# Performance work log

Measured on AMD Instinct MI355X. Metric: run time of the kernel, lower is better.

The kernel has to match this reference:

```python
import jax, jax.numpy as jnp
import numpy as np

B, T = 16, 1024
EMBED, HIDDEN = 128, 256
NUM_CLASSES, NUM_LABELS = 8000, 100


def setup_inputs() -> dict:
    key = jax.random.key(0)
    ks = jax.random.split(key, 9)
    s_in = 1.0 / np.sqrt(HIDDEN)  # PyTorch LSTMCell init: U(-1/sqrt(H), 1/sqrt(H))
    return {
        "x": jax.random.randint(ks[0], (B, T, 2), 0, NUM_LABELS, dtype=jnp.int64),
        "embed_x_w": jax.random.uniform(ks[1], (NUM_CLASSES, EMBED), jnp.float32, -0.1, 0.1),
        "embed_label_w": jax.random.uniform(ks[2], (NUM_LABELS, EMBED), jnp.float32, -0.1, 0.1),
        "W_ih": jax.random.uniform(ks[3], (4 * HIDDEN, 2 * EMBED), jnp.float32, -s_in, s_in),
        "W_hh": jax.random.uniform(ks[4], (4 * HIDDEN, HIDDEN), jnp.float32, -s_in, s_in),
        "b_ih": jax.random.uniform(ks[5], (4 * HIDDEN,), jnp.float32, -s_in, s_in),
        "b_hh": jax.random.uniform(ks[6], (4 * HIDDEN,), jnp.float32, -s_in, s_in),
        "fc_w": jax.random.uniform(ks[7], (NUM_CLASSES, HIDDEN), jnp.float32, -s_in, s_in),
        "fc_b": jax.random.uniform(ks[8], (NUM_CLASSES,), jnp.float32, -s_in, s_in),
    }


def _lstm_forward(x, embed_x_w, embed_label_w, W_ih, W_hh, b_ih, b_hh, fc_w, fc_b):
    H = W_hh.shape[1]
    # embedding lookups + concat: [B, T, 2E]
    x_emb = embed_x_w[x[:, :, 0]]
    l_emb = embed_label_w[x[:, :, 1]]
    inp = jnp.concatenate([x_emb, l_emb], axis=-1)
    # precompute input projection for all timesteps: [T, B, 4H]
    x_proj = jnp.einsum("bte,ge->tbg", inp, W_ih) + b_ih + b_hh

    def step(carry, xp_t):
        h, c = carry
        gates = xp_t + h @ W_hh.T  # [B, 4H]
        i = jax.nn.sigmoid(gates[:, 0 * H:1 * H])
        f = jax.nn.sigmoid(gates[:, 1 * H:2 * H])
        g = jnp.tanh(gates[:, 2 * H:3 * H])
        o = jax.nn.sigmoid(gates[:, 3 * H:4 * H])
        c_new = f * c + i * g
        h_new = o * jnp.tanh(c_new)
        return (h_new, c_new), h_new

    bsz = x.shape[0]
    h0 = jnp.zeros((bsz, H), x_proj.dtype)
    c0 = jnp.zeros((bsz, H), x_proj.dtype)
    _, hs = jax.lax.scan(step, (h0, c0), x_proj)  # hs: [T, B, H]
    hs = jnp.transpose(hs, (1, 0, 2))  # [B, T, H]
    return jnp.einsum("bth,ch->btc", hs, fc_w) + fc_b  # [B, T, C]


def reference(x, embed_x_w, embed_label_w, W_ih, W_hh, b_ih, b_hh, fc_w, fc_b):
    return _lstm_forward(x, embed_x_w, embed_label_w, W_ih, W_hh, b_ih, b_hh, fc_w, fc_b)
```

## Files before the change

### kernel.cpp

```cpp
#include <hip/hip_runtime.h>
#include <hip/hip_bf16.h>
#include <stdint.h>

#define B_ 16
#define T_ 1024
#define EMBED_ 128
#define HID_ 256
#define G4_ 1024
#define NC_ 8000
#define M_ (B_*T_)

typedef short bf16x8 __attribute__((ext_vector_type(8)));
typedef float f32x4 __attribute__((ext_vector_type(4)));

#if defined(__has_builtin)
#if __has_builtin(__builtin_amdgcn_sdot4)
#define SDOT4(a,b,c) __builtin_amdgcn_sdot4((a),(b),(c),false)
#endif
#endif
#ifndef SDOT4
__device__ __forceinline__ int sdot4_sw(int a, int b, int c) {
    c += (int)(signed char)(a)       * (int)(signed char)(b);
    c += (int)(signed char)(a >> 8)  * (int)(signed char)(b >> 8);
    c += (int)(signed char)(a >> 16) * (int)(signed char)(b >> 16);
    c += (int)(signed char)(a >> 24) * (int)(signed char)(b >> 24);
    return c;
}
#define SDOT4(a,b,c) sdot4_sw((a),(b),(c))
#endif

__device__ __forceinline__ float sigmoid_f(float x) {
    float e = __expf(-x);
    return __builtin_amdgcn_rcpf(1.f + e);
}

__global__ void embed_kernel(const int* __restrict__ x,
                             const float* __restrict__ ew,
                             const float* __restrict__ lw,
                             __hip_bfloat16* __restrict__ inp) {
    int m = blockIdx.x;
    int e = threadIdx.x;
    int i0 = x[2 * m];
    int i1 = x[2 * m + 1];
    float v = (e < EMBED_) ? ew[i0 * EMBED_ + e] : lw[i1 * EMBED_ + (e - EMBED_)];
    inp[m * 256 + e] = __float2bfloat16(v);
}

__global__ void f2bf_kernel(const float* __restrict__ in,
                            __hip_bfloat16* __restrict__ out, int n) {
    int i = blockIdx.x * blockDim.x + threadIdx.x;
    if (i < n) out[i] = __float2bfloat16(in[i]);
}

__global__ void quant_whh_kernel(const float* __restrict__ whh,
                                 int* __restrict__ wq, float* __restrict__ wscale) {
    int r = blockIdx.x;
    int lane = threadIdx.x;
    float4 v = ((const float4*)(whh + r * HID_))[lane];
    float m = fmaxf(fmaxf(fabsf(v.x), fabsf(v.y)), fmaxf(fabsf(v.z), fabsf(v.w)));
    #pragma unroll
    for (int off = 32; off; off >>= 1) m = fmaxf(m, __shfl_xor(m, off, 64));
    m = fmaxf(m, 1e-20f);
    float inv = 127.f / m;
    int q0 = __float2int_rn(v.x * inv) & 255;
    int q1 = __float2int_rn(v.y * inv) & 255;
    int q2 = __float2int_rn(v.z * inv) & 255;
    int q3 = __float2int_rn(v.w * inv) & 255;
    wq[r * 64 + lane] = q0 | (q1 << 8) | (q2 << 16) | (q3 << 24);
    if (lane == 0) wscale[r] = m * (1.f / 127.f);
}

__global__ __launch_bounds__(256, 4)
void gemm_bf16_kernel(const __hip_bfloat16* __restrict__ A,
                      const __hip_bfloat16* __restrict__ Bm,
                      const float* __restrict__ bias1,
                      const float* __restrict__ bias2,
                      float* __restrict__ C,
                      int N, int out_mode) {
    __shared__ short As[64][136];
    __shared__ short Bs[64][136];
    const int tid = threadIdx.x;
    const int m0 = blockIdx.y * 64;
    const int n0 = blockIdx.x * 64;
    const int w = tid >> 6;
    const int lane = tid & 63;
    const int l15 = lane & 15;
    const int q = lane >> 4;

    f32x4 zero4 = {0.f, 0.f, 0.f, 0.f};
    f32x4 acc[4] = {zero4, zero4, zero4, zero4};

    const int r = tid >> 2;
    const int cbase = tid & 3;

    for (int ko = 0; ko < 256; ko += 128) {
        #pragma unroll
        for (int i = 0; i < 4; ++i) {
            int c = cbase + (i << 2);
            uint4 av = ((const uint4*)A)[(size_t)(m0 + r) * 32 + (ko >> 3) + c];
            *((uint4*)&As[r][c * 8]) = av;
            uint4 bv = ((const uint4*)Bm)[(size_t)(n0 + r) * 32 + (ko >> 3) + c];
            *((uint4*)&Bs[r][c * 8]) = bv;
        }
        __syncthreads();
        #pragma unroll
        for (int kc = 0; kc < 4; ++kc) {
            bf16x8 af = *((const bf16x8*)&As[w * 16 + l15][kc * 32 + q * 8]);
            #pragma unroll
            for (int nt = 0; nt < 4; ++nt) {
                bf16x8 bfr = *((const bf16x8*)&Bs[nt * 16 + l15][kc * 32 + q * 8]);
                acc[nt] = __builtin_amdgcn_mfma_f32_16x16x32_bf16(af, bfr, acc[nt], 0, 0, 0);
            }
        }
        __syncthreads();
    }

    #pragma unroll
    for (int nt = 0; nt < 4; ++nt) {
        int n = n0 + nt * 16 + l15;
        float bsum = bias1[n] + (bias2 ? bias2[n] : 0.f);
        #pragma unroll
        for (int rg = 0; rg < 4; ++rg) {
            int m = m0 + w * 16 + q * 4 + rg;
            float val = acc[nt][rg] + bsum;
            if (out_mode == 0) {
                C[(size_t)m * N + n] = val;
            } else {
                int t = m & (T_ - 1), b = m >> 10;
                C[((size_t)((t << 4) + b) << 10) + n] = val;
            }
        }
    }
}

__global__ __launch_bounds__(512, 2)
void lstm_scan_kernel(const int* __restrict__ wq,
                      const float* __restrict__ wscale,
                      const float* __restrict__ xproj,
                      __hip_bfloat16* __restrict__ hs) {
    __shared__ __align__(16) int h_lds[2][64];

    const int tid = threadIdx.x;
    const int b = blockIdx.x;
    const int u = tid >> 1;
    const int odd = tid & 1;
    const int r0 = odd ? (256 + u) : u;
    const int r1 = odd ? (768 + u) : (512 + u);

    int w0[64], w1[64];
    {
        const int4* p0 = (const int4*)wq + r0 * 16;
        const int4* p1 = (const int4*)wq + r1 * 16;
        #pragma unroll
        for (int i = 0; i < 16; ++i) {
            int4 a = p0[i];
            w0[4 * i + 0] = a.x; w0[4 * i + 1] = a.y; w0[4 * i + 2] = a.z; w0[4 * i + 3] = a.w;
            int4 bb = p1[i];
            w1[4 * i + 0] = bb.x; w1[4 * i + 1] = bb.y; w1[4 * i + 2] = bb.z; w1[4 * i + 3] = bb.w;
        }
    }
    const float qs0 = wscale[r0] * (1.f / 127.f);
    const float qs1 = wscale[r1] * (1.f / 127.f);
    const float kb = odd ? 1.f : 2.f;
    const float mb = odd ? 1.f : 2.f;
    const float nb = odd ? 0.f : -1.f;

    if (tid < 64) h_lds[0][tid] = 0;
    float c = 0.f;
    float xp0 = xproj[(b << 10) + r0];
    float xp1 = xproj[(b << 10) + r1];
    __syncthreads();

    for (int t = 0; t < T_; ++t) {
        float nx0 = 0.f, nx1 = 0.f;
        if (t < T_ - 1) {
            const float* p = xproj + ((size_t)(((t + 1) << 4) + b) << 10);
            nx0 = p[r0];
            nx1 = p[r1];
        }
        int acc0 = 0, acc1 = 0;
        const int* hb = h_lds[t & 1];
        #pragma unroll
        for (int kd = 0; kd < 16; ++kd) {
            int4 hv = *((const int4*)(hb + kd * 4));
            acc0 = SDOT4(w0[4 * kd + 0], hv.x, acc0);
            acc0 = SDOT4(w0[4 * kd + 1], hv.y, acc0);
            acc0 = SDOT4(w0[4 * kd + 2], hv.z, acc0);
            acc0 = SDOT4(w0[4 * kd + 3], hv.w, acc0);
            acc1 = SDOT4(w1[4 * kd + 0], hv.x, acc1);
            acc1 = SDOT4(w1[4 * kd + 1], hv.y, acc1);
            acc1 = SDOT4(w1[4 * kd + 2], hv.z, acc1);
            acc1 = SDOT4(w1[4 * kd + 3], hv.w, acc1);
        }
        float ga = (float)acc0 * qs0 + xp0;
        float gb = (float)acc1 * qs1 + xp1;
        float a0 = sigmoid_f(ga);
        float a1 = sigmoid_f(kb * gb) * mb + nb;
        float pa0 = __shfl_xor(a0, 1, 64);
        float pa1 = __shfl_xor(a1, 1, 64);
        float iv = odd ? pa0 : a0;
        float fv = odd ? a0 : pa0;
        float gv = odd ? pa1 : a1;
        float ov = odd ? a1 : pa1;
        c = fv * c + iv * gv;
        float th = 2.f * sigmoid_f(c + c) - 1.f;
        float h = ov * th;
        if (!odd) {
            hs[(((size_t)(b << 10) + t) << 8) + u] = __float2bfloat16(h);
            ((signed char*)h_lds[(t + 1) & 1])[u] =
                (signed char)__float2int_rn(h * 127.f);
        }
        asm volatile("s_waitcnt lgkmcnt(0)" ::: "memory");
        __builtin_amdgcn_s_barrier();
        __builtin_amdgcn_sched_barrier(0);
        xp0 = nx0;
        xp1 = nx1;
    }
}

extern "C" void kernel_launch(void* const* d_in, const int* in_sizes, int n_in,
                              void* d_out, int out_size, void* d_ws, size_t ws_size,
                              hipStream_t stream) {
    const int* x            = (const int*)d_in[0];
    const float* embed_x_w  = (const float*)d_in[1];
    const float* embed_lb_w = (const float*)d_in[2];
    const float* W_ih       = (const float*)d_in[3];
    const float* W_hh       = (const float*)d_in[4];
    const float* b_ih       = (const float*)d_in[5];
    const float* b_hh       = (const float*)d_in[6];
    const float* fc_w       = (const float*)d_in[7];
    const float* fc_b       = (const float*)d_in[8];
    float* out = (float*)d_out;

    char* ws = (char*)d_ws;
    __hip_bfloat16* inp_bf = (__hip_bfloat16*)(ws);
    __hip_bfloat16* wih_bf = (__hip_bfloat16*)(ws + 8388608);
    __hip_bfloat16* fcw_bf = (__hip_bfloat16*)(ws + 8912896);
    int*   whh_q           = (int*)(ws + 13008896);
    float* whh_s           = (float*)(ws + 13271040);
    float* xproj           = (float*)(ws + 13275136);
    __hip_bfloat16* hs     = (__hip_bfloat16*)(ws + 80384000);
    (void)in_sizes; (void)n_in; (void)out_size; (void)ws_size;

    hipLaunchKernelGGL(embed_kernel, dim3(M_), dim3(256), 0, stream,
                       x, embed_x_w, embed_lb_w, inp_bf);
    hipLaunchKernelGGL(f2bf_kernel, dim3((G4_ * HID_ + 255) / 256), dim3(256), 0, stream,
                       W_ih, wih_bf, G4_ * HID_);
    hipLaunchKernelGGL(f2bf_kernel, dim3((NC_ * HID_ + 255) / 256), dim3(256), 0, stream,
                       fc_w, fcw_bf, NC_ * HID_);
    hipLaunchKernelGGL(quant_whh_kernel, dim3(G4_), dim3(64), 0, stream,
                       W_hh, whh_q, whh_s);
    hipLaunchKernelGGL(gemm_bf16_kernel, dim3(G4_ / 64, M_ / 64), dim3(256), 0, stream,
                       inp_bf, wih_bf, b_ih, b_hh, xproj, G4_, 1);
    hipLaunchKernelGGL(lstm_scan_kernel, dim3(B_), dim3(512), 0, stream,
                       whh_q, whh_s, xproj, hs);
    hipLaunchKernelGGL(gemm_bf16_kernel, dim3(NC_ / 64, M_ / 64), dim3(256), 0, stream,
                       hs, fcw_bf, fc_b, (const float*)nullptr, out, NC_, 0);
}
```

Measured before the change: 1.577 ms.

## Split LSTM scan to one gate row per thread with 1024-thread blocks

The recurrent scan kernel now uses 1024 threads per batch element, each owning a single gate row instead of two, which halves per-thread register weights and dot-product work per timestep. The four gates of a hidden unit are gathered with three xor shuffles instead of one, and the dot product is split into two independent accumulators to shorten the dependency chain. The aim is lower per-step latency on the serial recurrence. In exchange the per-step barrier now covers 16 wavefronts instead of 8, and each thread issues more shuffles and still performs the full 64-word LDS read of h.

```diff
diff --git a/kernel.cpp b/kernel.cpp
--- a/kernel.cpp
+++ b/kernel.cpp
@@ -133,7 +133,7 @@
     }
 }
 
-__global__ __launch_bounds__(512, 2)
+__global__ __launch_bounds__(1024, 4)
 void lstm_scan_kernel(const int* __restrict__ wq,
                       const float* __restrict__ wscale,
                       const float* __restrict__ xproj,
@@ -142,79 +142,78 @@
 
     const int tid = threadIdx.x;
     const int b = blockIdx.x;
-    const int u = tid >> 1;
-    const int odd = tid & 1;
-    const int r0 = odd ? (256 + u) : u;
-    const int r1 = odd ? (768 + u) : (512 + u);
-
-    int w0[64], w1[64];
+    const int j = tid & 3;
+    const int k = tid >> 2;
+    const int r = j * 256 + k;
+
+    int w[64];
     {
-        const int4* p0 = (const int4*)wq + r0 * 16;
-        const int4* p1 = (const int4*)wq + r1 * 16;
+        const int4* p = (const int4*)wq + r * 16;
         #pragma unroll
         for (int i = 0; i < 16; ++i) {
-            int4 a = p0[i];
-            w0[4 * i + 0] = a.x; w0[4 * i + 1] = a.y; w0[4 * i + 2] = a.z; w0[4 * i + 3] = a.w;
-            int4 bb = p1[i];
-            w1[4 * i + 0] = bb.x; w1[4 * i + 1] = bb.y; w1[4 * i + 2] = bb.z; w1[4 * i + 3] = bb.w;
-        }
-    }
-    const float qs0 = wscale[r0] * (1.f / 127.f);
-    const float qs1 = wscale[r1] * (1.f / 127.f);
-    const float kb = odd ? 1.f : 2.f;
-    const float mb = odd ? 1.f : 2.f;
-    const float nb = odd ? 0.f : -1.f;
+            int4 a = p[i];
+            w[4 * i + 0] = a.x; w[4 * i + 1] = a.y; w[4 * i + 2] = a.z; w[4 * i + 3] = a.w;
+        }
+    }
+    const float qs = wscale[r] * (1.f / 127.f);
+    const float kb = (j == 2) ? 2.f : 1.f;
+    const float nb = (j == 2) ? -1.f : 0.f;
+    const bool j1 = (j & 1) != 0;
+    const bool j2v = (j & 2) != 0;
 
     if (tid < 64) h_lds[0][tid] = 0;
     float c = 0.f;
-    float xp0 = xproj[(b << 10) + r0];
-    float xp1 = xproj[(b << 10) + r1];
+    float xp = xproj[(b << 10) + r];
     __syncthreads();
 
     for (int t = 0; t < T_; ++t) {
-        float nx0 = 0.f, nx1 = 0.f;
-        if (t < T_ - 1) {
-            const float* p = xproj + ((size_t)(((t + 1) << 4) + b) << 10);
-            nx0 = p[r0];
-            nx1 = p[r1];
-        }
+        float nx = 0.f;
+        if (t < T_ - 1) nx = xproj[(((size_t)(((t + 1) << 4) + b)) << 10) + r];
+
         int acc0 = 0, acc1 = 0;
         const int* hb = h_lds[t & 1];
         #pragma unroll
-        for (int kd = 0; kd < 16; ++kd) {
+        for (int kd = 0; kd < 8; ++kd) {
             int4 hv = *((const int4*)(hb + kd * 4));
-            acc0 = SDOT4(w0[4 * kd + 0], hv.x, acc0);
-            acc0 = SDOT4(w0[4 * kd + 1], hv.y, acc0);
-            acc0 = SDOT4(w0[4 * kd + 2], hv.z, acc0);
-            acc0 = SDOT4(w0[4 * kd + 3], hv.w, acc0);
-            acc1 = SDOT4(w1[4 * kd + 0], hv.x, acc1);
-            acc1 = SDOT4(w1[4 * kd + 1], hv.y, acc1);
-            acc1 = SDOT4(w1[4 * kd + 2], hv.z, acc1);
-            acc1 = SDOT4(w1[4 * kd + 3], hv.w, acc1);
-        }
-        float ga = (float)acc0 * qs0 + xp0;
-        float gb = (float)acc1 * qs1 + xp1;
-        float a0 = sigmoid_f(ga);
-        float a1 = sigmoid_f(kb * gb) * mb + nb;
-        float pa0 = __shfl_xor(a0, 1, 64);
-        float pa1 = __shfl_xor(a1, 1, 64);
-        float iv = odd ? pa0 : a0;
-        float fv = odd ? a0 : pa0;
-        float gv = odd ? pa1 : a1;
-        float ov = odd ? a1 : pa1;
+            acc0 = SDOT4(w[4 * kd + 0], hv.x, acc0);
+            acc1 = SDOT4(w[4 * kd + 1], hv.y, acc1);
+            acc0 = SDOT4(w[4 * kd + 2], hv.z, acc0);
+            acc1 = SDOT4(w[4 * kd + 3], hv.w, acc1);
+        }
+        #pragma unroll
+        for (int kd = 8; kd < 16; ++kd) {
+            int4 hv = *((const int4*)(hb + kd * 4));
+            acc0 = SDOT4(w[4 * kd + 0], hv.x, acc0);
+            acc1 = SDOT4(w[4 * kd + 1], hv.y, acc1);
+            acc0 = SDOT4(w[4 * kd + 2], hv.z, acc0);
+            acc1 = SDOT4(w[4 * kd + 3], hv.w, acc1);
+        }
+        float ga = (float)(acc0 + acc1) * qs + xp;
+        float a  = sigmoid_f(kb * ga) * kb + nb;
+
+        float e1 = __shfl_xor(a, 1, 64);
+        float e2 = __shfl_xor(a, 2, 64);
+        float e3 = __shfl_xor(a, 3, 64);
+        float s1a = j1 ? e1 : a;
+        float s1b = j1 ? a  : e1;
+        float s1c = j1 ? e3 : e2;
+        float s1d = j1 ? e2 : e3;
+        float iv = j2v ? s1c : s1a;
+        float fv = j2v ? s1d : s1b;
+        float gv = j2v ? s1a : s1c;
+        float ov = j2v ? s1b : s1d;
         c = fv * c + iv * gv;
         float th = 2.f * sigmoid_f(c + c) - 1.f;
         float h = ov * th;
-        if (!odd) {
-            hs[(((size_t)(b << 10) + t) << 8) + u] = __float2bfloat16(h);
-            ((signed char*)h_lds[(t + 1) & 1])[u] =
+        if (j == 0) {
+            hs[(((size_t)(b << 10) + t) << 8) + k] = __float2bfloat16(h);
+            ((signed char*)h_lds[(t + 1) & 1])[k] =
                 (signed char)__float2int_rn(h * 127.f);
         }
         asm volatile("s_waitcnt lgkmcnt(0)" ::: "memory");
         __builtin_amdgcn_s_barrier();
         __builtin_amdgcn_sched_barrier(0);
-        xp0 = nx0;
-        xp1 = nx1;
+        xp = nx;
     }
 }
 
@@ -252,7 +251,7 @@
                        W_hh, whh_q, whh_s);
     hipLaunchKernelGGL(gemm_bf16_kernel, dim3(G4_ / 64, M_ / 64), dim3(256), 0, stream,
                        inp_bf, wih_bf, b_ih, b_hh, xproj, G4_, 1);
-    hipLaunchKernelGGL(lstm_scan_kernel, dim3(B_), dim3(512), 0, stream,
+    hipLaunchKernelGGL(lstm_scan_kernel, dim3(B_), dim3(1024), 0, stream,
                        whh_q, whh_s, xproj, hs);
     hipLaunchKernelGGL(gemm_bf16_kernel, dim3(NC_ / 64, M_ / 64), dim3(256), 0, stream,
                        hs, fcw_bf, fc_b, (const float*)nullptr, out, NC_, 0);
```

Result: slower. 1.712 ms (+8.6%).
